# Optimization experiments

Measured on AMD Instinct MI355X. Metric: run time of the kernel, lower is better.

The kernel has to match this reference:

```python
import jax, jax.numpy as jnp
import numpy as np

NUM_LAYER = 5
EMB = 300
BN_EPS = 1e-5
NUM_BOND_TYPE = 6
NUM_BOND_DIR = 3
SELF_LOOP_TYPE = 4  # pretrain-gnns self-loop edge attr = [4, 0]


def setup_inputs() -> dict:
    key = jax.random.key(0)
    ks = jax.random.split(key, 12)
    N, E, D = 100000, 250000, EMB
    x = jax.random.normal(ks[0], (N, D), dtype=jnp.float32)
    edge_index = jax.random.randint(ks[1], (2, E), 0, N, dtype=jnp.int64)
    edge_attr = jax.random.randint(ks[2], (E, 2), 0, 3, dtype=jnp.int64)
    L = NUM_LAYER
    W1 = jax.random.normal(ks[3], (L, D, 2 * D), dtype=jnp.float32) * 0.05
    b1 = jnp.zeros((L, 2 * D), dtype=jnp.float32)
    W2 = jax.random.normal(ks[4], (L, 2 * D, D), dtype=jnp.float32) * 0.05
    b2 = jnp.zeros((L, D), dtype=jnp.float32)
    E1 = jax.random.normal(ks[5], (L, NUM_BOND_TYPE, D), dtype=jnp.float32) * 0.05
    E2 = jax.random.normal(ks[6], (L, NUM_BOND_DIR, D), dtype=jnp.float32) * 0.05
    gamma = jnp.ones((L, D), dtype=jnp.float32)
    beta = jnp.zeros((L, D), dtype=jnp.float32)
    return {"x": x, "edge_index": edge_index, "edge_attr": edge_attr,
            "W1": W1, "b1": b1, "W2": W2, "b2": b2,
            "E1": E1, "E2": E2, "gamma": gamma, "beta": beta}


def reference(x, edge_index, edge_attr, W1, b1, W2, b2, E1, E2, gamma, beta):
    N = x.shape[0]
    src, dst = edge_index[0], edge_index[1]
    bt, bd = edge_attr[:, 0], edge_attr[:, 1]
    h = x
    for l in range(NUM_LAYER):
        # GINEConv: message = x_j + edge_embedding, aggr='add', with self loops
        edge_emb = E1[l][bt] + E2[l][bd]                 # [E, D]
        self_emb = E1[l][SELF_LOOP_TYPE] + E2[l][0]      # [D]
        msg = h[src] + edge_emb                          # [E, D] gather
        agg = jax.ops.segment_sum(msg, dst, num_segments=N) + h + self_emb
        # update MLP: Linear(D,2D) -> ReLU -> Linear(2D,D)
        m = jax.nn.relu(agg @ W1[l] + b1[l]) @ W2[l] + b2[l]
        # BatchNorm1d in training mode (batch stats over nodes, biased var)
        mu = m.mean(axis=0)
        var = m.var(axis=0)
        m = (m - mu) * jax.lax.rsqrt(var + BN_EPS) * gamma[l] + beta[l]
        if l < NUM_LAYER - 1:  # ReLU on all but last layer; dropout ratio 0 -> no-op
            m = jax.nn.relu(m)
        h = m
    return h  # JK == 'last'
```

## Files before the change

kernel.cpp:

```cpp
#include <hip/hip_runtime.h>
#include <hip/hip_bf16.h>

#define NN 100000
#define NE 250000
#define DD 300
#define DDB 304
#define NL 5
#define MPAD 100096
#define KA1 320
#define N1 608
#define N1T 640
#define K2 608
#define N2T 384
#define NBLK 391
#define NCMB 19
#define XCHUNK 12512

typedef __attribute__((ext_vector_type(8))) short short8;
typedef __attribute__((ext_vector_type(4))) float f32x4;

#define GLBP(x) ((const __attribute__((address_space(1))) unsigned int*)(x))
#define LDSP(x) ((__attribute__((address_space(3))) unsigned int*)(x))
#define WAITV(N) asm volatile("s_waitcnt vmcnt(" #N ")" ::: "memory")

__device__ __forceinline__ ushort f2bf(float f){
  unsigned u = __float_as_uint(f);
  u += 0x7FFFu + ((u >> 16) & 1u);
  return (ushort)(u >> 16);
}
__device__ __forceinline__ float bf2f(ushort h){
  return __uint_as_float((unsigned)h << 16);
}
__device__ __forceinline__ unsigned pk2(float a, float b){
  return (unsigned)f2bf(a) | ((unsigned)f2bf(b) << 16);
}

__global__ void prep_weights(const float* __restrict__ W1, const float* __restrict__ W2,
                             ushort* __restrict__ W1T, ushort* __restrict__ W2T){
  int idx = blockIdx.x * 256 + threadIdx.x;
  const int total1 = NL * N1T * KA1;
  const int total2 = NL * N2T * K2;
  if (idx < total1){
    int l = idx / (N1T * KA1);
    int rem = idx % (N1T * KA1);
    int n = rem / KA1, k = rem % KA1;
    float v = (n < 2*DD && k < DD) ? W1[(size_t)l*DD*2*DD + (size_t)k*2*DD + n] : 0.0f;
    W1T[idx] = f2bf(v);
  } else {
    int idx2 = idx - total1;
    if (idx2 < total2){
      int l = idx2 / (N2T * K2);
      int rem = idx2 % (N2T * K2);
      int n = rem / K2, k = rem % K2;
      float v = (n < DD && k < 2*DD) ? W2[(size_t)l*2*DD*DD + (size_t)k*DD + n] : 0.0f;
      W2T[idx2] = f2bf(v);
    }
  }
}

__global__ void prep_ctab(const float* __restrict__ E1, const float* __restrict__ E2,
                          float* __restrict__ ctab){
  int idx = blockIdx.x * 256 + threadIdx.x;
  if (idx >= NL * NCMB * DDB) return;
  int l = idx / (NCMB * DDB);
  int rem = idx % (NCMB * DDB);
  int c = rem / DDB, d = rem % DDB;
  float v = 0.0f;
  if (d < DD){
    int bt = (c < 18) ? (c / 3) : 4;
    int bd = (c < 18) ? (c % 3) : 0;
    v = E1[(size_t)l*6*DD + bt*DD + d] + E2[(size_t)l*3*DD + bd*DD + d];
  }
  ctab[idx] = v;
}

__global__ void csr_count(const int* __restrict__ ei, int* __restrict__ deg){
  int e = blockIdx.x * 256 + threadIdx.x;
  if (e < NE) atomicAdd(&deg[ei[NE + e]], 1);
}

__global__ void scan_blk(const int* __restrict__ deg, int* __restrict__ rs, int* __restrict__ bsum){
  __shared__ int tmp[256];
  int i = blockIdx.x * 256 + threadIdx.x;
  int v = (i < NN) ? deg[i] : 0;
  tmp[threadIdx.x] = v;
  __syncthreads();
  #pragma unroll
  for (int off = 1; off < 256; off <<= 1){
    int t = (threadIdx.x >= off) ? tmp[threadIdx.x - off] : 0;
    __syncthreads();
    tmp[threadIdx.x] += t;
    __syncthreads();
  }
  if (i < NN) rs[i] = tmp[threadIdx.x] - v;
  if (threadIdx.x == 255) bsum[blockIdx.x] = tmp[255];
}

__global__ void scan_top(int* __restrict__ bsum){
  __shared__ int tmp[512];
  int v = (threadIdx.x < NBLK) ? bsum[threadIdx.x] : 0;
  tmp[threadIdx.x] = v;
  __syncthreads();
  #pragma unroll
  for (int off = 1; off < 512; off <<= 1){
    int t = (threadIdx.x >= off) ? tmp[threadIdx.x - off] : 0;
    __syncthreads();
    tmp[threadIdx.x] += t;
    __syncthreads();
  }
  if (threadIdx.x < NBLK) bsum[threadIdx.x] = tmp[threadIdx.x] - v;
}

__global__ void scan_add(int* __restrict__ rs, const int* __restrict__ bsum){
  int i = blockIdx.x * 256 + threadIdx.x;
  if (i < NN) rs[i] += bsum[blockIdx.x];
  if (i == 0) rs[NN] = NE;
}

__global__ void csr_fill(const int* __restrict__ ei, const int* __restrict__ ea,
                         const int* __restrict__ rs, int* __restrict__ cursor,
                         int* __restrict__ edges){
  int e = blockIdx.x * 256 + threadIdx.x;
  if (e < NE){
    int dst = ei[NE + e];
    int src = ei[e];
    int c = ea[2*e] * 3 + ea[2*e + 1];
    int p = rs[dst] + atomicAdd(&cursor[dst], 1);
    edges[p] = src | (c << 20);
  }
}

template<int HBF>
__global__ __launch_bounds__(256) void gather_agg(
    const void* __restrict__ hp, const float2* __restrict__ ss,
    const float* __restrict__ ctab_l,
    const int* __restrict__ rs, const int* __restrict__ edges,
    ushort* __restrict__ agg)
{
  int lane = threadIdx.x & 63;
  int wq = __builtin_amdgcn_readfirstlane(threadIdx.x >> 6);
  int xcd  = blockIdx.x & 7;
  int widx = (blockIdx.x >> 3) * 4 + wq;
  int rbeg = xcd * XCHUNK + widx;
  int rend = (xcd + 1) * XCHUNK;
  int dA = lane * 4;
  int dB = 256 + lane * 4;
  bool laneB  = (lane < 16);
  bool validB = (dB < DD);

  float scA[4], shA[4], scB[4], shB[4];
  if (HBF){
    #pragma unroll
    for (int j = 0; j < 4; ++j){
      float2 s = ss[dA + j]; scA[j] = s.x; shA[j] = s.y;
    }
    if (validB){
      #pragma unroll
      for (int j = 0; j < 4; ++j){
        float2 s = ss[dB + j]; scB[j] = s.x; shB[j] = s.y;
      }
    }
  }

  const float*  hf = (const float*)hp;
  const ushort* hb = (const ushort*)hp;
  const float* ctS = ctab_l + 18*DDB;

  for (int row = rbeg; row < rend; row += 512){
    float a0=0,a1=0,a2=0,a3=0, b0=0,b1v=0,b2v=0,b3=0;
    if (row < NN){
      if (HBF){
        uint2 hw = *(const uint2*)(hb + (size_t)row*DDB + dA);
        a0 = fmaxf(bf2f((ushort)hw.x)*scA[0]+shA[0],0.f)      + ctS[dA+0];
        a1 = fmaxf(bf2f((ushort)(hw.x>>16))*scA[1]+shA[1],0.f)+ ctS[dA+1];
        a2 = fmaxf(bf2f((ushort)hw.y)*scA[2]+shA[2],0.f)      + ctS[dA+2];
        a3 = fmaxf(bf2f((ushort)(hw.y>>16))*scA[3]+shA[3],0.f)+ ctS[dA+3];
        if (validB){
          uint2 hv = *(const uint2*)(hb + (size_t)row*DDB + dB);
          b0  = fmaxf(bf2f((ushort)hv.x)*scB[0]+shB[0],0.f)      + ctS[dB+0];
          b1v = fmaxf(bf2f((ushort)(hv.x>>16))*scB[1]+shB[1],0.f)+ ctS[dB+1];
          b2v = fmaxf(bf2f((ushort)hv.y)*scB[2]+shB[2],0.f)      + ctS[dB+2];
          b3  = fmaxf(bf2f((ushort)(hv.y>>16))*scB[3]+shB[3],0.f)+ ctS[dB+3];
        }
      } else {
        float4 hv = *(const float4*)(hf + (size_t)row*DD + dA);
        a0 = hv.x + ctS[dA+0]; a1 = hv.y + ctS[dA+1];
        a2 = hv.z + ctS[dA+2]; a3 = hv.w + ctS[dA+3];
        if (validB){
          float4 hv2 = *(const float4*)(hf + (size_t)row*DD + dB);
          b0 = hv2.x + ctS[dB+0]; b1v = hv2.y + ctS[dB+1];
          b2v = hv2.z + ctS[dB+2]; b3 = hv2.w + ctS[dB+3];
        }
      }
      int p = rs[row], pe = rs[row + 1];
      for (; p < pe; ++p){
        int ew = edges[p];
        int src = ew & 0xFFFFF;
        const float* ct = ctab_l + (ew >> 20)*DDB;
        if (HBF){
          uint2 hw = *(const uint2*)(hb + (size_t)src*DDB + dA);
          a0 += fmaxf(bf2f((ushort)hw.x)*scA[0]+shA[0],0.f)      + ct[dA+0];
          a1 += fmaxf(bf2f((ushort)(hw.x>>16))*scA[1]+shA[1],0.f)+ ct[dA+1];
          a2 += fmaxf(bf2f((ushort)hw.y)*scA[2]+shA[2],0.f)      + ct[dA+2];
          a3 += fmaxf(bf2f((ushort)(hw.y>>16))*scA[3]+shA[3],0.f)+ ct[dA+3];
          if (validB){
            uint2 hv = *(const uint2*)(hb + (size_t)src*DDB + dB);
            b0  += fmaxf(bf2f((ushort)hv.x)*scB[0]+shB[0],0.f)      + ct[dB+0];
            b1v += fmaxf(bf2f((ushort)(hv.x>>16))*scB[1]+shB[1],0.f)+ ct[dB+1];
            b2v += fmaxf(bf2f((ushort)hv.y)*scB[2]+shB[2],0.f)      + ct[dB+2];
            b3  += fmaxf(bf2f((ushort)(hv.y>>16))*scB[3]+shB[3],0.f)+ ct[dB+3];
          }
        } else {
          float4 hv = *(const float4*)(hf + (size_t)src*DD + dA);
          a0 += hv.x + ct[dA+0]; a1 += hv.y + ct[dA+1];
          a2 += hv.z + ct[dA+2]; a3 += hv.w + ct[dA+3];
          if (validB){
            float4 hv2 = *(const float4*)(hf + (size_t)src*DD + dB);
            b0 += hv2.x + ct[dB+0]; b1v += hv2.y + ct[dB+1];
            b2v += hv2.z + ct[dB+2]; b3 += hv2.w + ct[dB+3];
          }
        }
      }
    }
    ushort* ag = agg + (size_t)row*KA1;
    uint2 oA; oA.x = pk2(a0, a1); oA.y = pk2(a2, a3);
    *(uint2*)(ag + dA) = oA;
    if (laneB){
      uint2 oB;
      if (validB){ oB.x = pk2(b0, b1v); oB.y = pk2(b2v, b3); }
      else       { oB.x = 0; oB.y = 0; }
      *(uint2*)(ag + dB) = oB;
    }
  }
}

template<int OUT_BF16, int RELU, int STATS>
__global__ __launch_bounds__(512) void gemm_256(
    const ushort* __restrict__ A, int lda,
    const ushort* __restrict__ B, int ldb,
    void* __restrict__ Cp, int ldc,
    int kTiles, const float* __restrict__ bias, int biasN,
    int Mvalid, int Nvalid, int nColTiles, float* __restrict__ statf)
{
  __shared__ ushort As[3][8192];
  __shared__ ushort Bs[3][4096];
  int tid = threadIdx.x;
  int lane = tid & 63, w = tid >> 6;
  int wm = (w >> 1) * 64, wn = (w & 1) * 64;

  int nwg = gridDim.x;
  int q = nwg >> 3, r = nwg & 7;
  int xcd = blockIdx.x & 7, idx = blockIdx.x >> 3;
  int bid = (xcd < r ? xcd * (q + 1) : r * (q + 1) + (xcd - r) * q) + idx;
  int m0 = (bid / nColTiles) * 256;
  int n0 = (bid % nColTiles) * 128;

  int r0 = tid >> 2;
  int kc = ((tid & 3) ^ ((tid >> 3) & 3)) * 8;
  const ushort* Ap = A + (size_t)(m0 + r0)*lda + kc;
  const ushort* Bp = B + (size_t)(n0 + r0)*ldb + kc;

  f32x4 acc[4][4] = {};

#define STAGE(buf, kt) do { \
    int _ko = (kt) * 32; \
    __builtin_amdgcn_global_load_lds(GLBP(Ap + _ko),                   LDSP(&As[buf][w*512]),        16, 0, 0); \
    __builtin_amdgcn_global_load_lds(GLBP(Ap + _ko + (size_t)128*lda), LDSP(&As[buf][w*512 + 4096]), 16, 0, 0); \
    __builtin_amdgcn_global_load_lds(GLBP(Bp + _ko),                   LDSP(&Bs[buf][w*512]),        16, 0, 0); \
  } while (0)

  STAGE(0, 0);
  STAGE(1, 1);
  WAITV(3);
  __builtin_amdgcn_s_barrier();

  int fr = lane & 15;
  int ko8 = (((lane >> 4) ^ ((fr >> 1) & 3))) * 8;
  int cur = 0;
  for (int kt = 0; kt < kTiles; ++kt){
    int sb = cur + 2; if (sb >= 3) sb -= 3;
    if (kt + 2 < kTiles) STAGE(sb, kt + 2);
    short8 af[4], bfv[4];
    #pragma unroll
    for (int i = 0; i < 4; ++i)
      af[i] = *(const short8*)&As[cur][(wm + i*16 + fr)*32 + ko8];
    #pragma unroll
    for (int j = 0; j < 4; ++j)
      bfv[j] = *(const short8*)&Bs[cur][(wn + j*16 + fr)*32 + ko8];
    #pragma unroll
    for (int i = 0; i < 4; ++i)
      #pragma unroll
      for (int j = 0; j < 4; ++j)
        acc[i][j] = __builtin_amdgcn_mfma_f32_16x16x32_bf16(af[i], bfv[j], acc[i][j], 0, 0, 0);
    if (kt + 1 < kTiles){
      if (kt + 2 < kTiles) WAITV(3);
      else                 WAITV(0);
      __builtin_amdgcn_s_barrier();
    }
    cur = cur + 1; if (cur >= 3) cur = 0;
  }
#undef STAGE

  int cc = lane & 15, cr = (lane >> 4) * 4;
  float ps[4], pq[4];
  if (STATS){
    #pragma unroll
    for (int j = 0; j < 4; ++j){ ps[j] = 0.0f; pq[j] = 0.0f; }
  }
  #pragma unroll
  for (int i = 0; i < 4; ++i){
    #pragma unroll
    for (int j = 0; j < 4; ++j){
      int col = n0 + wn + j*16 + cc;
      if (col >= Nvalid) continue;
      float bv = (col < biasN) ? bias[col] : 0.0f;
      #pragma unroll
      for (int r2 = 0; r2 < 4; ++r2){
        int row = m0 + wm + i*16 + cr + r2;
        if (row < Mvalid){
          float v = acc[i][j][r2] + bv;
          if (RELU) v = fmaxf(v, 0.0f);
          if (OUT_BF16) ((ushort*)Cp)[(size_t)row*ldc + col] = f2bf(v);
          else          ((float*) Cp)[(size_t)row*ldc + col] = v;
          if (STATS){ ps[j] += v; pq[j] += v * v; }
        }
      }
    }
  }
  if (STATS){
    #pragma unroll
    for (int j = 0; j < 4; ++j){
      float s = ps[j], qv = pq[j];
      s += __shfl_xor(s, 16); qv += __shfl_xor(qv, 16);
      s += __shfl_xor(s, 32); qv += __shfl_xor(qv, 32);
      int col = n0 + wn + j*16 + cc;
      if ((lane >> 4) == 0 && col < Nvalid){
        unsafeAtomicAdd(&statf[col], s);
        unsafeAtomicAdd(&statf[N2T + col], qv);
      }
    }
  }
}

__global__ void make_norm(const float* __restrict__ statf, const float* __restrict__ gamma,
                          const float* __restrict__ beta, float2* __restrict__ ss){
  int d = threadIdx.x;
  if (d >= DD) return;
  double mu = (double)statf[d] / (double)NN;
  double var = (double)statf[N2T + d] / (double)NN - mu * mu;
  float inv = rsqrtf((float)var + 1e-5f);
  float sc = inv * gamma[d];
  ss[d] = make_float2(sc, beta[d] - (float)mu * sc);
}

__global__ void apply_norm(const float* __restrict__ m2, const float2* __restrict__ ss,
                           float* __restrict__ out){
  int row = blockIdx.x;
  int d = threadIdx.x;
  if (d >= DD) return;
  float2 s = ss[d];
  out[(size_t)row*DD + d] = m2[(size_t)row*DD + d] * s.x + s.y;
}

extern "C" void kernel_launch(void* const* d_in, const int* in_sizes, int n_in,
                              void* d_out, int out_size, void* d_ws, size_t ws_size,
                              hipStream_t stream) {
  const float* x     = (const float*)d_in[0];
  const int*   ei    = (const int*)  d_in[1];
  const int*   ea    = (const int*)  d_in[2];
  const float* W1    = (const float*)d_in[3];
  const float* b1    = (const float*)d_in[4];
  const float* W2    = (const float*)d_in[5];
  const float* b2    = (const float*)d_in[6];
  const float* E1    = (const float*)d_in[7];
  const float* E2    = (const float*)d_in[8];
  const float* gamma = (const float*)d_in[9];
  const float* beta  = (const float*)d_in[10];

  char* p = (char*)d_ws;
  float*  m2buf = (float*) p; p += (size_t)NN * DD * 4;
  ushort* m2bf  = (ushort*)p; p += (size_t)NN * DDB * 2;
  ushort* agg   = (ushort*)p; p += (size_t)MPAD * KA1 * 2;
  ushort* m1    = (ushort*)p; p += (size_t)MPAD * N1 * 2;
  ushort* W1T   = (ushort*)p; p += (size_t)NL * N1T * KA1 * 2;
  ushort* W2T   = (ushort*)p; p += (size_t)NL * N2T * K2 * 2;
  float*  ctab  = (float*) p; p += (size_t)NL * NCMB * DDB * 4;
  int*    deg   = (int*)   p; p += (size_t)NN * 4;
  int*    rs    = (int*)   p; p += (size_t)(NN + 16) * 4;
  int*    bsum  = (int*)   p; p += (size_t)512 * 4;
  int*    cursor= (int*)   p; p += (size_t)NN * 4;
  int*    edges = (int*)   p; p += (size_t)NE * 4;
  float*  statf = (float*) p; p += (size_t)2 * N2T * 4;
  float2* ss    = (float2*)p;

  {
    int total = NL*N1T*KA1 + NL*N2T*K2;
    prep_weights<<<(total + 255)/256, 256, 0, stream>>>(W1, W2, W1T, W2T);
    int tc = NL * NCMB * DDB;
    prep_ctab<<<(tc + 255)/256, 256, 0, stream>>>(E1, E2, ctab);
  }
  hipMemsetAsync(deg, 0, (size_t)NN*4, stream);
  hipMemsetAsync(cursor, 0, (size_t)NN*4, stream);
  csr_count<<<(NE + 255)/256, 256, 0, stream>>>(ei, deg);
  scan_blk<<<NBLK, 256, 0, stream>>>(deg, rs, bsum);
  scan_top<<<1, 512, 0, stream>>>(bsum);
  scan_add<<<NBLK, 256, 0, stream>>>(rs, bsum);
  csr_fill<<<(NE + 255)/256, 256, 0, stream>>>(ei, ea, rs, cursor, edges);

  for (int l = 0; l < NL; ++l){
    const float* ctab_l = ctab + (size_t)l * NCMB * DDB;

    if (l == 0)
      gather_agg<0><<<1024, 256, 0, stream>>>(x, nullptr, ctab_l, rs, edges, agg);
    else
      gather_agg<1><<<1024, 256, 0, stream>>>(m2bf, ss, ctab_l, rs, edges, agg);

    gemm_256<1,1,0><<<(MPAD/256) * (N1T/128), 512, 0, stream>>>(
        agg, KA1, W1T + (size_t)l*N1T*KA1, KA1, m1, N1, KA1/32,
        b1 + (size_t)l*2*DD, 2*DD, MPAD, N1, N1T/128, nullptr);

    hipMemsetAsync(statf, 0, (size_t)2*N2T*4, stream);

    if (l < NL - 1)
      gemm_256<1,0,1><<<(MPAD/256) * (N2T/128), 512, 0, stream>>>(
          m1, N1, W2T + (size_t)l*N2T*K2, K2, m2bf, DDB, K2/32,
          b2 + (size_t)l*DD, DD, NN, DD, N2T/128, statf);
    else
      gemm_256<0,0,1><<<(MPAD/256) * (N2T/128), 512, 0, stream>>>(
          m1, N1, W2T + (size_t)l*N2T*K2, K2, m2buf, DD, K2/32,
          b2 + (size_t)l*DD, DD, NN, DD, N2T/128, statf);

    make_norm<<<1, 320, 0, stream>>>(statf, gamma + (size_t)l*DD, beta + (size_t)l*DD, ss);
  }
  apply_norm<<<NN, 320, 0, stream>>>(m2buf, ss, (float*)d_out);
}
```

Before: 1.524 ms.

## Replace pipelined LDS GEMM with persistent B-resident GEMM streaming A from registers

Swaps the 256x128 tiled GEMM, which triple-buffered A and B tiles through LDS, for a persistent kernel. Each block loads a 64-column slab of the transposed weight into padded LDS once, then loops over its XCD's 256-row tiles, loading A fragments straight from global memory into registers with a 4-deep prefetch. This removes the per-k-tile barriers and the repeated staging of B. It also regroups row tiles by XCD so A reads stay local to each XCD's cache. The cost is more register pressure, no LDS reuse of A across the N dimension, and smaller 64-wide N slabs, so A is reread from global memory once per slab.

New measurement: 3.500 ms. 2.3x slower.

```diff
diff --git a/kernel.cpp b/kernel.cpp
--- a/kernel.cpp
+++ b/kernel.cpp
@@ -14,14 +14,11 @@
 #define N2T 384
 #define NBLK 391
 #define NCMB 19
-#define XCHUNK 12512
+#define TPX 49
+#define XCHUNK 12544
 
 typedef __attribute__((ext_vector_type(8))) short short8;
 typedef __attribute__((ext_vector_type(4))) float f32x4;
-
-#define GLBP(x) ((const __attribute__((address_space(1))) unsigned int*)(x))
-#define LDSP(x) ((__attribute__((address_space(3))) unsigned int*)(x))
-#define WAITV(N) asm volatile("s_waitcnt vmcnt(" #N ")" ::: "memory")
 
 __device__ __forceinline__ ushort f2bf(float f){
   unsigned u = __float_as_uint(f);
@@ -142,7 +139,7 @@
   int xcd  = blockIdx.x & 7;
   int widx = (blockIdx.x >> 3) * 4 + wq;
   int rbeg = xcd * XCHUNK + widx;
-  int rend = (xcd + 1) * XCHUNK;
+  int rend = min((xcd + 1) * XCHUNK, MPAD);
   int dA = lane * 4;
   int dB = 256 + lane * 4;
   bool laneB  = (lane < 16);
@@ -234,109 +231,113 @@
   }
 }
 
-template<int OUT_BF16, int RELU, int STATS>
-__global__ __launch_bounds__(512) void gemm_256(
+template<int KTILES, int KROW, int KPAD, int NSLABS, int SUBS,
+         int OUT_BF16, int RELU, int STATS>
+__global__ __launch_bounds__(256) void gemm_bfree(
     const ushort* __restrict__ A, int lda,
-    const ushort* __restrict__ B, int ldb,
+    const ushort* __restrict__ BT,
     void* __restrict__ Cp, int ldc,
-    int kTiles, const float* __restrict__ bias, int biasN,
-    int Mvalid, int Nvalid, int nColTiles, float* __restrict__ statf)
+    const float* __restrict__ bias, int biasN,
+    int Mvalid, int Nvalid, float* __restrict__ statf)
 {
-  __shared__ ushort As[3][8192];
-  __shared__ ushort Bs[3][4096];
+  __shared__ ushort Bs[64 * KPAD];
   int tid = threadIdx.x;
   int lane = tid & 63, w = tid >> 6;
-  int wm = (w >> 1) * 64, wn = (w & 1) * 64;
-
-  int nwg = gridDim.x;
-  int q = nwg >> 3, r = nwg & 7;
-  int xcd = blockIdx.x & 7, idx = blockIdx.x >> 3;
-  int bid = (xcd < r ? xcd * (q + 1) : r * (q + 1) + (xcd - r) * q) + idx;
-  int m0 = (bid / nColTiles) * 256;
-  int n0 = (bid % nColTiles) * 128;
-
-  int r0 = tid >> 2;
-  int kc = ((tid & 3) ^ ((tid >> 3) & 3)) * 8;
-  const ushort* Ap = A + (size_t)(m0 + r0)*lda + kc;
-  const ushort* Bp = B + (size_t)(n0 + r0)*ldb + kc;
-
-  f32x4 acc[4][4] = {};
-
-#define STAGE(buf, kt) do { \
-    int _ko = (kt) * 32; \
-    __builtin_amdgcn_global_load_lds(GLBP(Ap + _ko),                   LDSP(&As[buf][w*512]),        16, 0, 0); \
-    __builtin_amdgcn_global_load_lds(GLBP(Ap + _ko + (size_t)128*lda), LDSP(&As[buf][w*512 + 4096]), 16, 0, 0); \
-    __builtin_amdgcn_global_load_lds(GLBP(Bp + _ko),                   LDSP(&Bs[buf][w*512]),        16, 0, 0); \
-  } while (0)
-
-  STAGE(0, 0);
-  STAGE(1, 1);
-  WAITV(3);
-  __builtin_amdgcn_s_barrier();
-
-  int fr = lane & 15;
-  int ko8 = (((lane >> 4) ^ ((fr >> 1) & 3))) * 8;
-  int cur = 0;
-  for (int kt = 0; kt < kTiles; ++kt){
-    int sb = cur + 2; if (sb >= 3) sb -= 3;
-    if (kt + 2 < kTiles) STAGE(sb, kt + 2);
-    short8 af[4], bfv[4];
+  int xcd = blockIdx.x & 7;
+  int v = blockIdx.x >> 3;
+  int slab = v % NSLABS;
+  int sub  = v / NSLABS;
+  int n0 = slab * 64;
+
+  {
+    const ushort* src = BT + (size_t)n0 * KROW;
+    const int CPR = KROW / 8;
+    #pragma unroll
+    for (int c2 = 0; c2 < (64 * KROW / 8) / 256; ++c2){
+      int c = c2 * 256 + tid;
+      int row = c / CPR;
+      int ko  = (c % CPR) * 8;
+      uint4 val = *(const uint4*)(src + (size_t)row * KROW + ko);
+      *(uint4*)&Bs[row * KPAD + ko] = val;
+    }
+  }
+  __syncthreads();
+
+  int fr = lane & 15, kq = lane >> 4;
+  int cr = kq * 4;
+  int tbeg = xcd * TPX;
+  int tend = min(tbeg + TPX, NBLK);
+
+  for (int mt = tbeg + sub; mt < tend; mt += SUBS){
+    int m0 = mt * 256 + w * 64;
+    const ushort* Ar[4];
     #pragma unroll
     for (int i = 0; i < 4; ++i)
-      af[i] = *(const short8*)&As[cur][(wm + i*16 + fr)*32 + ko8];
-    #pragma unroll
-    for (int j = 0; j < 4; ++j)
-      bfv[j] = *(const short8*)&Bs[cur][(wn + j*16 + fr)*32 + ko8];
-    #pragma unroll
-    for (int i = 0; i < 4; ++i)
+      Ar[i] = A + (size_t)(m0 + i*16 + fr) * lda + kq * 8;
+
+    f32x4 acc[4][4] = {};
+    short8 ap[4][4];
+
+    #pragma unroll
+    for (int t = 0; t < 4; ++t)
+      #pragma unroll
+      for (int i = 0; i < 4; ++i)
+        ap[t][i] = *(const short8*)(Ar[i] + t*32);
+
+    #pragma unroll
+    for (int kt = 0; kt < KTILES; ++kt){
+      short8 bf[4];
       #pragma unroll
       for (int j = 0; j < 4; ++j)
-        acc[i][j] = __builtin_amdgcn_mfma_f32_16x16x32_bf16(af[i], bfv[j], acc[i][j], 0, 0, 0);
-    if (kt + 1 < kTiles){
-      if (kt + 2 < kTiles) WAITV(3);
-      else                 WAITV(0);
-      __builtin_amdgcn_s_barrier();
-    }
-    cur = cur + 1; if (cur >= 3) cur = 0;
-  }
-#undef STAGE
-
-  int cc = lane & 15, cr = (lane >> 4) * 4;
-  float ps[4], pq[4];
-  if (STATS){
-    #pragma unroll
-    for (int j = 0; j < 4; ++j){ ps[j] = 0.0f; pq[j] = 0.0f; }
-  }
-  #pragma unroll
-  for (int i = 0; i < 4; ++i){
-    #pragma unroll
-    for (int j = 0; j < 4; ++j){
-      int col = n0 + wn + j*16 + cc;
-      if (col >= Nvalid) continue;
-      float bv = (col < biasN) ? bias[col] : 0.0f;
-      #pragma unroll
-      for (int r2 = 0; r2 < 4; ++r2){
-        int row = m0 + wm + i*16 + cr + r2;
-        if (row < Mvalid){
-          float v = acc[i][j][r2] + bv;
-          if (RELU) v = fmaxf(v, 0.0f);
-          if (OUT_BF16) ((ushort*)Cp)[(size_t)row*ldc + col] = f2bf(v);
-          else          ((float*) Cp)[(size_t)row*ldc + col] = v;
-          if (STATS){ ps[j] += v; pq[j] += v * v; }
+        bf[j] = *(const short8*)&Bs[(j*16 + fr)*KPAD + kt*32 + kq*8];
+      #pragma unroll
+      for (int i = 0; i < 4; ++i)
+        #pragma unroll
+        for (int j = 0; j < 4; ++j)
+          acc[i][j] = __builtin_amdgcn_mfma_f32_16x16x32_bf16(ap[kt & 3][i], bf[j], acc[i][j], 0, 0, 0);
+      if (kt + 4 < KTILES){
+        #pragma unroll
+        for (int i = 0; i < 4; ++i)
+          ap[kt & 3][i] = *(const short8*)(Ar[i] + (kt + 4)*32);
+      }
+    }
+
+    float ps[4], pq[4];
+    if (STATS){
+      #pragma unroll
+      for (int j = 0; j < 4; ++j){ ps[j] = 0.0f; pq[j] = 0.0f; }
+    }
+    #pragma unroll
+    for (int i = 0; i < 4; ++i){
+      #pragma unroll
+      for (int j = 0; j < 4; ++j){
+        int col = n0 + j*16 + fr;
+        if (col >= Nvalid) continue;
+        float bv = (col < biasN) ? bias[col] : 0.0f;
+        #pragma unroll
+        for (int r2 = 0; r2 < 4; ++r2){
+          int row = m0 + i*16 + cr + r2;
+          if (row < Mvalid){
+            float val = acc[i][j][r2] + bv;
+            if (RELU) val = fmaxf(val, 0.0f);
+            if (OUT_BF16) ((ushort*)Cp)[(size_t)row*ldc + col] = f2bf(val);
+            else          ((float*) Cp)[(size_t)row*ldc + col] = val;
+            if (STATS){ ps[j] += val; pq[j] += val * val; }
+          }
         }
       }
     }
-  }
-  if (STATS){
-    #pragma unroll
-    for (int j = 0; j < 4; ++j){
-      float s = ps[j], qv = pq[j];
-      s += __shfl_xor(s, 16); qv += __shfl_xor(qv, 16);
-      s += __shfl_xor(s, 32); qv += __shfl_xor(qv, 32);
-      int col = n0 + wn + j*16 + cc;
-      if ((lane >> 4) == 0 && col < Nvalid){
-        unsafeAtomicAdd(&statf[col], s);
-        unsafeAtomicAdd(&statf[N2T + col], qv);
+    if (STATS){
+      #pragma unroll
+      for (int j = 0; j < 4; ++j){
+        float s = ps[j], qv = pq[j];
+        s += __shfl_xor(s, 16); qv += __shfl_xor(qv, 16);
+        s += __shfl_xor(s, 32); qv += __shfl_xor(qv, 32);
+        int col = n0 + j*16 + fr;
+        if (kq == 0 && col < Nvalid){
+          unsafeAtomicAdd(&statf[col], s);
+          unsafeAtomicAdd(&statf[N2T + col], qv);
+        }
       }
     }
   }
@@ -415,20 +416,20 @@
     else
       gather_agg<1><<<1024, 256, 0, stream>>>(m2bf, ss, ctab_l, rs, edges, agg);
 
-    gemm_256<1,1,0><<<(MPAD/256) * (N1T/128), 512, 0, stream>>>(
-        agg, KA1, W1T + (size_t)l*N1T*KA1, KA1, m1, N1, KA1/32,
-        b1 + (size_t)l*2*DD, 2*DD, MPAD, N1, N1T/128, nullptr);
+    gemm_bfree<10, KA1, 344, 10, 7, 1, 1, 0><<<8*10*7, 256, 0, stream>>>(
+        agg, KA1, W1T + (size_t)l*N1T*KA1, m1, N1,
+        b1 + (size_t)l*2*DD, 2*DD, MPAD, N1, nullptr);
 
     hipMemsetAsync(statf, 0, (size_t)2*N2T*4, stream);
 
     if (l < NL - 1)
-      gemm_256<1,0,1><<<(MPAD/256) * (N2T/128), 512, 0, stream>>>(
-          m1, N1, W2T + (size_t)l*N2T*K2, K2, m2bf, DDB, K2/32,
-          b2 + (size_t)l*DD, DD, NN, DD, N2T/128, statf);
+      gemm_bfree<19, K2, 616, 5, 12, 1, 0, 1><<<8*5*12, 256, 0, stream>>>(
+          m1, N1, W2T + (size_t)l*N2T*K2, m2bf, DDB,
+          b2 + (size_t)l*DD, DD, NN, DD, statf);
     else
-      gemm_256<0,0,1><<<(MPAD/256) * (N2T/128), 512, 0, stream>>>(
-          m1, N1, W2T + (size_t)l*N2T*K2, K2, m2buf, DD, K2/32,
-          b2 + (size_t)l*DD, DD, NN, DD, N2T/128, statf);
+      gemm_bfree<19, K2, 616, 5, 12, 0, 0, 1><<<8*5*12, 256, 0, stream>>>(
+          m1, N1, W2T + (size_t)l*N2T*K2, m2buf, DD,
+          b2 + (size_t)l*DD, DD, NN, DD, statf);
 
     make_norm<<<1, 320, 0, stream>>>(statf, gamma + (size_t)l*DD, beta + (size_t)l*DD, ss);
   }
```

## Load GEMM B fragments directly to registers and double gather grid

Applied to the files above, without the earlier changes.

The GEMM kernel no longer stages the weight (B) tile through LDS. Each wave loads its B fragments straight from global memory into registers, one k-tile ahead, while A keeps the three-buffer LDS pipeline. This removes the LDS traffic and footprint for B, but the B loads are now redundant across the four waves that share columns, and the vmcnt accounting gets harder. Separately, the gather kernel launches twice as many blocks, with its row stride derived from the grid size, to raise occupancy.

New measurement: 1.853 ms. +21.6%, slower.

```diff
diff --git a/kernel.cpp b/kernel.cpp
--- a/kernel.cpp
+++ b/kernel.cpp
@@ -141,6 +141,7 @@
   int wq = __builtin_amdgcn_readfirstlane(threadIdx.x >> 6);
   int xcd  = blockIdx.x & 7;
   int widx = (blockIdx.x >> 3) * 4 + wq;
+  int nwX  = (gridDim.x >> 3) * 4;
   int rbeg = xcd * XCHUNK + widx;
   int rend = (xcd + 1) * XCHUNK;
   int dA = lane * 4;
@@ -166,7 +167,7 @@
   const ushort* hb = (const ushort*)hp;
   const float* ctS = ctab_l + 18*DDB;
 
-  for (int row = rbeg; row < rend; row += 512){
+  for (int row = rbeg; row < rend; row += nwX){
     float a0=0,a1=0,a2=0,a3=0, b0=0,b1v=0,b2v=0,b3=0;
     if (row < NN){
       if (HBF){
@@ -235,7 +236,7 @@
 }
 
 template<int OUT_BF16, int RELU, int STATS>
-__global__ __launch_bounds__(512) void gemm_256(
+__global__ __launch_bounds__(512) void gemm_256_bd(
     const ushort* __restrict__ A, int lda,
     const ushort* __restrict__ B, int ldb,
     void* __restrict__ Cp, int ldc,
@@ -243,7 +244,6 @@
     int Mvalid, int Nvalid, int nColTiles, float* __restrict__ statf)
 {
   __shared__ ushort As[3][8192];
-  __shared__ ushort Bs[3][4096];
   int tid = threadIdx.x;
   int lane = tid & 63, w = tid >> 6;
   int wm = (w >> 1) * 64, wn = (w & 1) * 64;
@@ -258,50 +258,60 @@
   int r0 = tid >> 2;
   int kc = ((tid & 3) ^ ((tid >> 3) & 3)) * 8;
   const ushort* Ap = A + (size_t)(m0 + r0)*lda + kc;
-  const ushort* Bp = B + (size_t)(n0 + r0)*ldb + kc;
+
+  int fr = lane & 15, kq = lane >> 4;
+  int ko8 = ((kq ^ ((fr >> 1) & 3))) * 8;
+  const ushort* Bl = B + (size_t)(n0 + wn + fr)*ldb + kq*8;
 
   f32x4 acc[4][4] = {};
-
-#define STAGE(buf, kt) do { \
+  short8 bcur[4], bnext[4];
+
+#define STAGE_A(buf, kt) do { \
     int _ko = (kt) * 32; \
     __builtin_amdgcn_global_load_lds(GLBP(Ap + _ko),                   LDSP(&As[buf][w*512]),        16, 0, 0); \
     __builtin_amdgcn_global_load_lds(GLBP(Ap + _ko + (size_t)128*lda), LDSP(&As[buf][w*512 + 4096]), 16, 0, 0); \
-    __builtin_amdgcn_global_load_lds(GLBP(Bp + _ko),                   LDSP(&Bs[buf][w*512]),        16, 0, 0); \
   } while (0)
 
-  STAGE(0, 0);
-  STAGE(1, 1);
-  WAITV(3);
+  STAGE_A(0, 0);
+  #pragma unroll
+  for (int j = 0; j < 4; ++j)
+    bcur[j] = *(const short8*)(Bl + (size_t)j*16*ldb);
+  STAGE_A(1, 1);
+  WAITV(2);
   __builtin_amdgcn_s_barrier();
 
-  int fr = lane & 15;
-  int ko8 = (((lane >> 4) ^ ((fr >> 1) & 3))) * 8;
   int cur = 0;
   for (int kt = 0; kt < kTiles; ++kt){
     int sb = cur + 2; if (sb >= 3) sb -= 3;
-    if (kt + 2 < kTiles) STAGE(sb, kt + 2);
-    short8 af[4], bfv[4];
+    int issued = 0;
+    if (kt + 2 < kTiles){ STAGE_A(sb, kt + 2); issued += 2; }
+    if (kt + 1 < kTiles){
+      #pragma unroll
+      for (int j = 0; j < 4; ++j)
+        bnext[j] = *(const short8*)(Bl + (size_t)j*16*ldb + (kt + 1)*32);
+      issued += 4;
+    }
+    short8 af[4];
     #pragma unroll
     for (int i = 0; i < 4; ++i)
       af[i] = *(const short8*)&As[cur][(wm + i*16 + fr)*32 + ko8];
-    #pragma unroll
-    for (int j = 0; j < 4; ++j)
-      bfv[j] = *(const short8*)&Bs[cur][(wn + j*16 + fr)*32 + ko8];
     #pragma unroll
     for (int i = 0; i < 4; ++i)
       #pragma unroll
       for (int j = 0; j < 4; ++j)
-        acc[i][j] = __builtin_amdgcn_mfma_f32_16x16x32_bf16(af[i], bfv[j], acc[i][j], 0, 0, 0);
+        acc[i][j] = __builtin_amdgcn_mfma_f32_16x16x32_bf16(af[i], bcur[j], acc[i][j], 0, 0, 0);
     if (kt + 1 < kTiles){
-      if (kt + 2 < kTiles) WAITV(3);
-      else                 WAITV(0);
+      if (issued == 6)      WAITV(6);
+      else                  WAITV(4);
       __builtin_amdgcn_s_barrier();
+      #pragma unroll
+      for (int j = 0; j < 4; ++j) bcur[j] = bnext[j];
     }
     cur = cur + 1; if (cur >= 3) cur = 0;
   }
-#undef STAGE
-
-  int cc = lane & 15, cr = (lane >> 4) * 4;
+#undef STAGE_A
+
+  int cc = lane & 15, cr = kq * 4;
   float ps[4], pq[4];
   if (STATS){
     #pragma unroll
@@ -334,7 +344,7 @@
       s += __shfl_xor(s, 16); qv += __shfl_xor(qv, 16);
       s += __shfl_xor(s, 32); qv += __shfl_xor(qv, 32);
       int col = n0 + wn + j*16 + cc;
-      if ((lane >> 4) == 0 && col < Nvalid){
+      if (kq == 0 && col < Nvalid){
         unsafeAtomicAdd(&statf[col], s);
         unsafeAtomicAdd(&statf[N2T + col], qv);
       }
@@ -411,22 +421,22 @@
     const float* ctab_l = ctab + (size_t)l * NCMB * DDB;
 
     if (l == 0)
-      gather_agg<0><<<1024, 256, 0, stream>>>(x, nullptr, ctab_l, rs, edges, agg);
+      gather_agg<0><<<2048, 256, 0, stream>>>(x, nullptr, ctab_l, rs, edges, agg);
     else
-      gather_agg<1><<<1024, 256, 0, stream>>>(m2bf, ss, ctab_l, rs, edges, agg);
-
-    gemm_256<1,1,0><<<(MPAD/256) * (N1T/128), 512, 0, stream>>>(
+      gather_agg<1><<<2048, 256, 0, stream>>>(m2bf, ss, ctab_l, rs, edges, agg);
+
+    gemm_256_bd<1,1,0><<<(MPAD/256) * (N1T/128), 512, 0, stream>>>(
         agg, KA1, W1T + (size_t)l*N1T*KA1, KA1, m1, N1, KA1/32,
         b1 + (size_t)l*2*DD, 2*DD, MPAD, N1, N1T/128, nullptr);
 
     hipMemsetAsync(statf, 0, (size_t)2*N2T*4, stream);
 
     if (l < NL - 1)
-      gemm_256<1,0,1><<<(MPAD/256) * (N2T/128), 512, 0, stream>>>(
+      gemm_256_bd<1,0,1><<<(MPAD/256) * (N2T/128), 512, 0, stream>>>(
           m1, N1, W2T + (size_t)l*N2T*K2, K2, m2bf, DDB, K2/32,
           b2 + (size_t)l*DD, DD, NN, DD, N2T/128, statf);
     else
-      gemm_256<0,0,1><<<(MPAD/256) * (N2T/128), 512, 0, stream>>>(
+      gemm_256_bd<0,0,1><<<(MPAD/256) * (N2T/128), 512, 0, stream>>>(
           m1, N1, W2T + (size_t)l*N2T*K2, K2, m2buf, DD, K2/32,
           b2 + (size_t)l*DD, DD, NN, DD, N2T/128, statf);
 
```
